# Kernel tuning notes

Measured on AMD Instinct MI355X. Metric: run time of the kernel, lower is better.

## Reference

```python
import jax, jax.numpy as jnp
import numpy as np

EPS = 1e-5

def batchnorm(x, g, b):
    # training-mode BN: batch statistics over (N,H,W), biased variance (matches torch)
    m = x.mean((0, 2, 3), keepdims=True)
    v = ((x - m) ** 2).mean((0, 2, 3), keepdims=True)
    return g[None, :, None, None] * (x - m) * jax.lax.rsqrt(v + EPS) + b[None, :, None, None]


def deform_conv2d(x, offset, mask, weight, bias):
    # torchvision deform_conv2d v2 semantics, stride=1, pad=1, dilation=1, 1 group, 1 offset group
    B, C, H, W = x.shape
    K = 9  # 3x3 kernel
    off = offset.reshape(B, K, 2, H, W)  # interleaved (dy, dx) per kernel tap
    dy, dx = off[:, :, 0], off[:, :, 1]  # [B,K,H,W]
    kr = jnp.arange(3, dtype=x.dtype) - 1.0
    k_y = jnp.repeat(kr, 3)  # [9] kernel row offsets
    k_x = jnp.tile(kr, 3)    # [9] kernel col offsets
    hh = jnp.arange(H, dtype=x.dtype)
    ww = jnp.arange(W, dtype=x.dtype)
    ph = dy + k_y[None, :, None, None] + hh[None, None, :, None]  # [B,K,H,W] sample rows
    pw = dx + k_x[None, :, None, None] + ww[None, None, None, :]  # [B,K,H,W] sample cols
    h0 = jnp.floor(ph); w0 = jnp.floor(pw)
    lh = ph - h0; lw = pw - w0
    h0i = h0.astype(jnp.int32); w0i = w0.astype(jnp.int32)

    def gather(xb, hb, wb):  # xb [C,H,W], hb/wb [K,H,W] -> [C,K,H,W]
        return xb[:, hb, wb]

    def corner(hi, wi, wgt):
        valid = (hi >= 0) & (hi < H) & (wi >= 0) & (wi < W)
        hic = jnp.clip(hi, 0, H - 1); wic = jnp.clip(wi, 0, W - 1)
        v = jax.vmap(gather)(x, hic, wic)  # [B,C,K,H,W]
        return v * (wgt * valid.astype(x.dtype))[:, None]

    samp = (corner(h0i, w0i, (1 - lh) * (1 - lw))
            + corner(h0i, w0i + 1, (1 - lh) * lw)
            + corner(h0i + 1, w0i, lh * (1 - lw))
            + corner(h0i + 1, w0i + 1, lh * lw))  # [B,C,K,H,W]
    samp = samp * mask[:, None]  # modulated (v2) mask [B,1,K,H,W]
    out = jnp.einsum('bckhw,ock->bohw', samp, weight.reshape(weight.shape[0], C, K))
    return out + bias[None, :, None, None]


def reference(x, conv1_w, bn1_g, bn1_b, off_w, off_b, dcn_w, dcn_b, norm_g, norm_b):
    flip = x[..., ::-1]
    xp = batchnorm(jnp.einsum('bchw,oc->bohw', x, conv1_w), bn1_g, bn1_b)  # 1x1 conv + BN, no relu
    concat = jnp.concatenate([flip, xp], axis=1)  # [B,2C,H,W]
    out = jax.lax.conv_general_dilated(concat, off_w, (1, 1), 'SAME',
                                       dimension_numbers=('NCHW', 'OIHW', 'NCHW'))
    out = out + off_b[None, :, None, None]  # [B,27,H,W]
    o1, o2, mask = jnp.split(out, 3, axis=1)
    offset = jnp.concatenate([o1, o2], axis=1)  # [B,18,H,W]
    mask = jax.nn.sigmoid(mask)  # [B,9,H,W]
    d = deform_conv2d(xp, offset, mask, dcn_w, dcn_b)
    return jax.nn.relu(batchnorm(d, norm_g, norm_b) + xp)


def setup_inputs() -> dict:
    key = jax.random.key(0)
    ks = jax.random.split(key, 6)
    B, C, H, W = 8, 256, 45, 80
    stdv = 1.0 / np.sqrt(C * 9)
    return {
        'x': jax.random.normal(ks[0], (B, C, H, W), jnp.float32),
        'conv1_w': jax.random.normal(ks[1], (C, C), jnp.float32) * 0.05,
        'bn1_g': jnp.ones((C,), jnp.float32),
        'bn1_b': jnp.zeros((C,), jnp.float32),
        'off_w': jax.random.normal(ks[2], (27, 2 * C, 3, 3), jnp.float32) * 0.01,
        'off_b': jax.random.normal(ks[3], (27,), jnp.float32) * 0.01,
        'dcn_w': jax.random.uniform(ks[4], (C, C, 3, 3), jnp.float32, -stdv, stdv),
        'dcn_b': jax.random.normal(ks[5], (C,), jnp.float32) * 0.01,
        'norm_g': jnp.ones((C,), jnp.float32),
        'norm_b': jnp.zeros((C,), jnp.float32),
    }
```

## Files before the change

kernel.cpp:

```cpp
#include <hip/hip_runtime.h>
#include <math.h>

#define BATCH 8
#define CH 256
#define HH 45
#define WW 80
#define HW 3600
#define PTOT 28800

typedef unsigned short u16;
typedef unsigned int   u32;
typedef __attribute__((ext_vector_type(8))) short bf16x8;
typedef __attribute__((ext_vector_type(4))) float f32x4;

struct __align__(8) us4 { u16 x, y, z, w; };

__device__ __forceinline__ u16 bf16_rne(float x) {
  u32 u = __float_as_uint(x);
  u += 0x7FFF + ((u >> 16) & 1);
  return (u16)(u >> 16);
}

__global__ __launch_bounds__(256) void prep_wts(
    const float* __restrict__ conv1_w, const float* __restrict__ off_w,
    const float* __restrict__ dcn_w,
    u16* __restrict__ w1b, u16* __restrict__ wt_offb, u16* __restrict__ wt_b)
{
  int i = blockIdx.x * 256 + threadIdx.x;
  if (i < 256 * 256) {
    w1b[i] = bf16_rne(conv1_w[i]);
  }
  if (i < 9 * 32 * 512) {
    int tap = i >> 14;
    int r   = i & 16383;
    int oc  = r >> 9;
    int c   = r & 511;
    float v = (oc < 27) ? off_w[((size_t)oc * 512 + c) * 9 + tap] : 0.f;
    wt_offb[i] = bf16_rne(v);
  }
  if (i < 9 * 256 * 256) {
    int c = i & 255;
    int oc = (i >> 8) & 255;
    int tap = i >> 16;
    wt_b[i] = bf16_rne(dcn_w[((size_t)oc * 256 + c) * 9 + tap]);
  }
}

__global__ __launch_bounds__(256) void flip_transpose(
    const float* __restrict__ x, u16* __restrict__ concat)
{
  __shared__ float tile[32][36];
  const int b  = blockIdx.z;
  const int c0 = blockIdx.y * 32;
  const int p0 = blockIdx.x * 32;
  int rem = HW - p0; if (rem > 32) rem = 32;
  const int t = threadIdx.x;
  {
    int c = t >> 3, p4 = (t & 7) * 4;
    if (p4 < rem) {
      float4 v = *(const float4*)(x + ((size_t)b * CH + c0 + c) * HW + p0 + p4);
      *(float4*)&tile[c][p4] = v;
    }
  }
  __syncthreads();
  {
    int r = t >> 3, cq = (t & 7) * 4;
    if (r < rem) {
      int p = p0 + r;
      int h = p / WW, w = p - h * WW;
      int pf = h * WW + (WW - 1 - w);
      us4 o;
      o.x = bf16_rne(tile[cq + 0][r]);
      o.y = bf16_rne(tile[cq + 1][r]);
      o.z = bf16_rne(tile[cq + 2][r]);
      o.w = bf16_rne(tile[cq + 3][r]);
      *(us4*)(concat + ((size_t)b * HW + pf) * 512 + c0 + cq) = o;
    }
  }
}

__global__ __launch_bounds__(256) void conv1_mfma(
    const u16* __restrict__ concat, const u16* __restrict__ w1b,
    float* __restrict__ out1, float* __restrict__ part_c1)
{
  const int t = threadIdx.x;
  const int wv = t >> 6, lane = t & 63;
  const int lr = lane & 15, lk = lane >> 4;
  const int id = blockIdx.x;
  const int b  = id & 7;
  const int pt = id >> 3;
  const int oc0 = blockIdx.y * 128 + (wv & 1) * 64;
  const int p0  = pt * 128 + (wv >> 1) * 64;

  const u16* bptr[4];
#pragma unroll
  for (int nt = 0; nt < 4; nt++) {
    int pl = p0 + nt * 16 + lr;
    int pc = pl < HW ? pl : HW - 1;
    int h = pc / WW, w = pc - h * WW;
    int pf = b * HW + h * WW + (WW - 1 - w);
    bptr[nt] = concat + (size_t)pf * 512 + lk * 8;
  }
  const u16* aptr = w1b + ((size_t)(oc0 + lr)) * 256 + lk * 8;

  f32x4 acc[4][4];
#pragma unroll
  for (int mt = 0; mt < 4; mt++)
#pragma unroll
    for (int nt = 0; nt < 4; nt++) acc[mt][nt] = (f32x4)0.f;

#pragma unroll
  for (int cc = 0; cc < 8; cc++) {
    bf16x8 af[4], bfv[4];
#pragma unroll
    for (int mt = 0; mt < 4; mt++)
      af[mt] = *(const bf16x8*)(aptr + (size_t)mt * 16 * 256 + cc * 32);
#pragma unroll
    for (int nt = 0; nt < 4; nt++)
      bfv[nt] = *(const bf16x8*)(bptr[nt] + cc * 32);
#pragma unroll
    for (int mt = 0; mt < 4; mt++)
#pragma unroll
      for (int nt = 0; nt < 4; nt++)
        acc[mt][nt] = __builtin_amdgcn_mfma_f32_16x16x32_bf16(
            af[mt], bfv[nt], acc[mt][nt], 0, 0, 0);
  }

#pragma unroll
  for (int mt = 0; mt < 4; mt++) {
    int oc = oc0 + mt * 16 + lk * 4;
#pragma unroll
    for (int nt = 0; nt < 4; nt++) {
      int pl = p0 + nt * 16 + lr;
      if (pl < HW) {
        float* dst = out1 + ((size_t)(b * CH + oc)) * HW + pl;
#pragma unroll
        for (int r = 0; r < 4; r++)
          dst[(size_t)r * HW] = acc[mt][nt][r];
      }
    }
  }

  float sv[4][4], sq[4][4];
#pragma unroll
  for (int mt = 0; mt < 4; mt++)
#pragma unroll
    for (int r = 0; r < 4; r++) { sv[mt][r] = 0.f; sq[mt][r] = 0.f; }
#pragma unroll
  for (int mt = 0; mt < 4; mt++)
#pragma unroll
    for (int nt = 0; nt < 4; nt++) {
      int pl = p0 + nt * 16 + lr;
      if (pl < HW) {
#pragma unroll
        for (int r = 0; r < 4; r++) {
          float v = acc[mt][nt][r];
          sv[mt][r] += v; sq[mt][r] += v * v;
        }
      }
    }
#pragma unroll
  for (int m = 1; m < 16; m <<= 1) {
#pragma unroll
    for (int mt = 0; mt < 4; mt++)
#pragma unroll
      for (int r = 0; r < 4; r++) {
        sv[mt][r] += __shfl_xor(sv[mt][r], m, 64);
        sq[mt][r] += __shfl_xor(sq[mt][r], m, 64);
      }
  }
  if (lr == 0) {
    int slot = (wv >> 1) + 2 * blockIdx.x + 464 * blockIdx.y;
    float* pp = part_c1 + (size_t)slot * 128 * 2;
#pragma unroll
    for (int mt = 0; mt < 4; mt++)
#pragma unroll
      for (int r = 0; r < 4; r++) {
        int ocl = (wv & 1) * 64 + mt * 16 + lk * 4 + r;
        pp[ocl * 2]     = sv[mt][r];
        pp[ocl * 2 + 1] = sq[mt][r];
      }
  }
}

__global__ __launch_bounds__(256) void stats_fin_c1(
    const float* __restrict__ part_c1, float* __restrict__ st)
{
  const int c = blockIdx.x;
  const int y = c >> 7, ocl = c & 127;
  const int t = threadIdx.x;
  const float* base = part_c1 + (size_t)y * 464 * 256 + ocl * 2;
  float s = 0.f, s2 = 0.f;
  for (int i = t; i < 464; i += 256) {
    s  += base[(size_t)i * 256];
    s2 += base[(size_t)i * 256 + 1];
  }
  __shared__ float ls[256], ls2[256];
  ls[t] = s; ls2[t] = s2;
  __syncthreads();
  for (int off = 128; off > 0; off >>= 1) {
    if (t < off) { ls[t] += ls[t + off]; ls2[t] += ls2[t + off]; }
    __syncthreads();
  }
  if (t == 0) {
    float m = ls[0] / (float)PTOT;
    float var = ls2[0] / (float)PTOT - m * m;
    st[c] = m;
    st[CH + c] = rsqrtf(var + 1e-5f);
  }
}

__global__ __launch_bounds__(256) void stats_fin_d(
    const float* __restrict__ part_d, float* __restrict__ st)
{
  const int c = blockIdx.x;
  const int t = threadIdx.x;
  float s = 0.f, s2 = 0.f;
  for (int i = t; i < 456; i += 256) {
    s  += part_d[(size_t)i * 512 + c * 2];
    s2 += part_d[(size_t)i * 512 + c * 2 + 1];
  }
  __shared__ float ls[256], ls2[256];
  ls[t] = s; ls2[t] = s2;
  __syncthreads();
  for (int off = 128; off > 0; off >>= 1) {
    if (t < off) { ls[t] += ls[t + off]; ls2[t] += ls2[t + off]; }
    __syncthreads();
  }
  if (t == 0) {
    float m = ls[0] / (float)PTOT;
    float var = ls2[0] / (float)PTOT - m * m;
    st[c] = m;
    st[CH + c] = rsqrtf(var + 1e-5f);
  }
}

__global__ __launch_bounds__(256) void norm_transpose(
    const float* __restrict__ out1, const float* __restrict__ st,
    const float* __restrict__ g, const float* __restrict__ bb,
    u16* __restrict__ concat)
{
  __shared__ float tile[32][36];
  const int b  = blockIdx.z;
  const int c0 = blockIdx.y * 32;
  const int p0 = blockIdx.x * 32;
  int rem = HW - p0; if (rem > 32) rem = 32;
  const int t = threadIdx.x;

  {
    int c  = t >> 3;
    int p4 = (t & 7) * 4;
    int cg = c0 + c;
    float m  = st[cg], rs = st[CH + cg];
    float sc = g[cg] * rs;
    float sh = bb[cg] - m * sc;
    if (p4 < rem) {
      size_t base = ((size_t)b * CH + cg) * HW + p0;
      float4 v = *(const float4*)(out1 + base + p4);
      v.x = v.x * sc + sh; v.y = v.y * sc + sh;
      v.z = v.z * sc + sh; v.w = v.w * sc + sh;
      *(float4*)&tile[c][p4] = v;
    }
  }
  __syncthreads();
  {
    int r  = t >> 3;
    int cq = (t & 7) * 4;
    if (r < rem) {
      us4 o;
      o.x = bf16_rne(tile[cq + 0][r]);
      o.y = bf16_rne(tile[cq + 1][r]);
      o.z = bf16_rne(tile[cq + 2][r]);
      o.w = bf16_rne(tile[cq + 3][r]);
      *(us4*)(concat + ((size_t)b * HW + p0 + r) * 512 + 256 + c0 + cq) = o;
    }
  }
}

__global__ __launch_bounds__(128) void off_mfma(
    const u16* __restrict__ concat, const u16* __restrict__ wt_offb,
    float* __restrict__ offp3)
{
  const int t = threadIdx.x;
  const int g = blockIdx.y;
  const int wv = t >> 6, lane = t & 63;
  const int lr = lane & 15, lk = lane >> 4;
  const int id = blockIdx.x;
  const int b    = id & 7;
  const int tile = id >> 3;
  int pl = tile * 32 + wv * 16 + lr;
  const bool pvalid = pl < HW;
  if (!pvalid) pl = HW - 1;
  const int P = b * HW + pl;
  const int h = pl / WW, w = pl - h * WW;

  f32x4 acc[2];
  acc[0] = (f32x4)0.f; acc[1] = (f32x4)0.f;

#pragma unroll 1
  for (int tl = 0; tl < 3; tl++) {
    int tap = g * 3 + tl;
    int dy = tap / 3 - 1, dx = tap % 3 - 1;
    bool valid = ((unsigned)(h + dy) < HH) && ((unsigned)(w + dx) < WW);
    int Ps = valid ? (P + dy * WW + dx) : P;
    const u16* bp = concat + (size_t)Ps * 512 + lk * 8;
    const u16* ap = wt_offb + ((size_t)tap * 32 + lr) * 512 + lk * 8;
#pragma unroll
    for (int cc = 0; cc < 16; cc++) {
      bf16x8 bfv = *(const bf16x8*)(bp + cc * 32);
      if (!valid) bfv = (bf16x8)(short)0;
      bf16x8 af0 = *(const bf16x8*)(ap + cc * 32);
      bf16x8 af1 = *(const bf16x8*)(ap + 16 * 512 + cc * 32);
      acc[0] = __builtin_amdgcn_mfma_f32_16x16x32_bf16(af0, bfv, acc[0], 0, 0, 0);
      acc[1] = __builtin_amdgcn_mfma_f32_16x16x32_bf16(af1, bfv, acc[1], 0, 0, 0);
    }
  }

  if (pvalid) {
#pragma unroll
    for (int mt = 0; mt < 2; mt++) {
      int oc = mt * 16 + lk * 4;
#pragma unroll
      for (int r = 0; r < 4; r++)
        offp3[((size_t)g * 32 + oc + r) * PTOT + P] = acc[mt][r];
    }
  }
}

__global__ __launch_bounds__(256) void off_finalize(
    const float* __restrict__ offp3, const float* __restrict__ off_b,
    float4* __restrict__ wts4, int4* __restrict__ idx4)
{
  int i = blockIdx.x * 256 + threadIdx.x;
  if (i >= 9 * PTOT) return;
  int k = i / PTOT;
  int P = i - k * PTOT;
  int b = P / HW;
  int p = P - b * HW;
  int h = p / WW;
  int w = p - h * WW;

  float dy = off_b[2 * k], dx = off_b[2 * k + 1], ml = off_b[18 + k];
#pragma unroll
  for (int g = 0; g < 3; g++) {
    const float* base = offp3 + (size_t)g * 32 * PTOT + P;
    dy += base[(size_t)(2 * k    ) * PTOT];
    dx += base[(size_t)(2 * k + 1) * PTOT];
    ml += base[(size_t)(18 + k   ) * PTOT];
  }

  float m = 1.f / (1.f + expf(-ml));
  float ph = dy + (float)(k / 3 - 1) + (float)h;
  float pw = dx + (float)(k % 3 - 1) + (float)w;
  float h0f = floorf(ph), w0f = floorf(pw);
  float lh = ph - h0f, lw = pw - w0f;
  int h0 = (int)h0f, w0 = (int)w0f;
  int h1 = h0 + 1, w1 = w0 + 1;
  float vh0 = (h0 >= 0 && h0 < HH) ? 1.f : 0.f;
  float vh1 = (h1 >= 0 && h1 < HH) ? 1.f : 0.f;
  float vw0 = (w0 >= 0 && w0 < WW) ? 1.f : 0.f;
  float vw1 = (w1 >= 0 && w1 < WW) ? 1.f : 0.f;
  float4 wv;
  wv.x = (1.f - lh) * (1.f - lw) * m * vh0 * vw0;
  wv.y = (1.f - lh) * lw         * m * vh0 * vw1;
  wv.z = lh * (1.f - lw)         * m * vh1 * vw0;
  wv.w = lh * lw                 * m * vh1 * vw1;
  int hc0 = min(max(h0, 0), HH - 1), hc1 = min(max(h1, 0), HH - 1);
  int wc0 = min(max(w0, 0), WW - 1), wc1 = min(max(w1, 0), WW - 1);
  int base = b * HW;
  int4 iv;
  iv.x = (base + hc0 * WW + wc0) * 512 + 256;
  iv.y = (base + hc0 * WW + wc1) * 512 + 256;
  iv.z = (base + hc1 * WW + wc0) * 512 + 256;
  iv.w = (base + hc1 * WW + wc1) * 512 + 256;
  wts4[i] = wv;
  idx4[i] = iv;
}

__global__ __launch_bounds__(512) void deform_mfma(
    const u16* __restrict__ concat,
    const float4* __restrict__ wts4, const int4* __restrict__ idx4,
    const u16* __restrict__ wt_b,
    float* __restrict__ d, float* __restrict__ part_d)
{
  __shared__ u16   samp[64 * 256];
  __shared__ float4 sw4[64];
  __shared__ int4   sidx4[64];

  const int t    = threadIdx.x;
  const int wv   = t >> 6;
  const int lane = t & 63;
  const int lr = lane & 15, lk = lane >> 4;
  const int id   = blockIdx.x;
  const int b    = id & 7;
  const int tile = id >> 3;
  const int P0   = b * HW + tile * 64;
  int lim  = HW - tile * 64;
  if (lim > 64) lim = 64;

  f32x4 acc[2][4];
#pragma unroll
  for (int mt = 0; mt < 2; mt++)
#pragma unroll
    for (int nt = 0; nt < 4; nt++) acc[mt][nt] = (f32x4)0.f;

  const int c4 = lane * 4;

  for (int tap = 0; tap < 9; tap++) {
    __syncthreads();
    if (t < 64) {
      int off = (t < lim) ? t : (lim - 1);
      sw4[t]   = wts4[(size_t)tap * PTOT + P0 + off];
      sidx4[t] = idx4[(size_t)tap * PTOT + P0 + off];
    }
    __syncthreads();

#pragma unroll 2
    for (int it = 0; it < 8; it++) {
      int pos = it * 8 + wv;
      int4  iv = sidx4[pos];
      float4 wq = sw4[pos];
      uint2 u0 = *(const uint2*)(concat + iv.x + c4);
      uint2 u1 = *(const uint2*)(concat + iv.y + c4);
      uint2 u2 = *(const uint2*)(concat + iv.z + c4);
      uint2 u3 = *(const uint2*)(concat + iv.w + c4);
      float a0, a1, a2, a3;
      a0  = wq.x * __uint_as_float(u0.x << 16);
      a1  = wq.x * __uint_as_float(u0.x & 0xFFFF0000u);
      a2  = wq.x * __uint_as_float(u0.y << 16);
      a3  = wq.x * __uint_as_float(u0.y & 0xFFFF0000u);
      a0 = fmaf(wq.y, __uint_as_float(u1.x << 16), a0);
      a1 = fmaf(wq.y, __uint_as_float(u1.x & 0xFFFF0000u), a1);
      a2 = fmaf(wq.y, __uint_as_float(u1.y << 16), a2);
      a3 = fmaf(wq.y, __uint_as_float(u1.y & 0xFFFF0000u), a3);
      a0 = fmaf(wq.z, __uint_as_float(u2.x << 16), a0);
      a1 = fmaf(wq.z, __uint_as_float(u2.x & 0xFFFF0000u), a1);
      a2 = fmaf(wq.z, __uint_as_float(u2.y << 16), a2);
      a3 = fmaf(wq.z, __uint_as_float(u2.y & 0xFFFF0000u), a3);
      a0 = fmaf(wq.w, __uint_as_float(u3.x << 16), a0);
      a1 = fmaf(wq.w, __uint_as_float(u3.x & 0xFFFF0000u), a1);
      a2 = fmaf(wq.w, __uint_as_float(u3.y << 16), a2);
      a3 = fmaf(wq.w, __uint_as_float(u3.y & 0xFFFF0000u), a3);
      uint2 r;
      r.x = (__float_as_uint(a0) >> 16) | (__float_as_uint(a1) & 0xFFFF0000u);
      r.y = (__float_as_uint(a2) >> 16) | (__float_as_uint(a3) & 0xFFFF0000u);
      u32 byte = (u32)pos * 512u + (u32)c4 * 2u;
      byte ^= (u32)(pos & 7) << 4;
      *(uint2*)((char*)samp + byte) = r;
    }
    __syncthreads();

#pragma unroll 1
    for (int cc = 0; cc < 8; cc++) {
      int c0 = cc * 32;
      bf16x8 bfr[4];
#pragma unroll
      for (int nt = 0; nt < 4; nt++) {
        int pos = nt * 16 + lr;
        u32 byte = (u32)pos * 512u + (u32)(c0 + lk * 8) * 2u;
        byte ^= (u32)(pos & 7) << 4;
        bfr[nt] = *(const bf16x8*)((const char*)samp + byte);
      }
      const u16* wp = wt_b + ((size_t)tap * 256 + wv * 32 + lr) * 256
                      + c0 + lk * 8;
      bf16x8 afr[2];
#pragma unroll
      for (int mt = 0; mt < 2; mt++)
        afr[mt] = *(const bf16x8*)(wp + (size_t)mt * 16 * 256);
#pragma unroll
      for (int mt = 0; mt < 2; mt++)
#pragma unroll
        for (int nt = 0; nt < 4; nt++)
          acc[mt][nt] = __builtin_amdgcn_mfma_f32_16x16x32_bf16(
              afr[mt], bfr[nt], acc[mt][nt], 0, 0, 0);
    }
  }

#pragma unroll
  for (int mt = 0; mt < 2; mt++) {
    int oc = wv * 32 + mt * 16 + lk * 4;
#pragma unroll
    for (int nt = 0; nt < 4; nt++) {
      int pl = tile * 64 + nt * 16 + lr;
      if (pl < HW) {
        float* dst = d + ((size_t)(b * CH + oc)) * HW + pl;
#pragma unroll
        for (int r = 0; r < 4; r++)
          dst[(size_t)r * HW] = acc[mt][nt][r];
      }
    }
  }

  float sv[2][4], sq[2][4];
#pragma unroll
  for (int mt = 0; mt < 2; mt++)
#pragma unroll
    for (int r = 0; r < 4; r++) { sv[mt][r] = 0.f; sq[mt][r] = 0.f; }
#pragma unroll
  for (int mt = 0; mt < 2; mt++)
#pragma unroll
    for (int nt = 0; nt < 4; nt++) {
      int pl = tile * 64 + nt * 16 + lr;
      if (pl < HW) {
#pragma unroll
        for (int r = 0; r < 4; r++) {
          float v = acc[mt][nt][r];
          sv[mt][r] += v; sq[mt][r] += v * v;
        }
      }
    }
#pragma unroll
  for (int m = 1; m < 16; m <<= 1) {
#pragma unroll
    for (int mt = 0; mt < 2; mt++)
#pragma unroll
      for (int r = 0; r < 4; r++) {
        sv[mt][r] += __shfl_xor(sv[mt][r], m, 64);
        sq[mt][r] += __shfl_xor(sq[mt][r], m, 64);
      }
  }
  if (lr == 0) {
    float* pp = part_d + (size_t)blockIdx.x * 512;
#pragma unroll
    for (int mt = 0; mt < 2; mt++)
#pragma unroll
      for (int r = 0; r < 4; r++) {
        int oc = wv * 32 + mt * 16 + lk * 4 + r;
        pp[oc * 2]     = sv[mt][r];
        pp[oc * 2 + 1] = sq[mt][r];
      }
  }
}

__global__ __launch_bounds__(256) void final_nchw(
    const float* __restrict__ d, const float* __restrict__ out1raw,
    const float* __restrict__ st1, const float* __restrict__ g1,
    const float* __restrict__ b1,
    const float* __restrict__ st2, const float* __restrict__ g2,
    const float* __restrict__ b2, float* __restrict__ out)
{
  u32 i4 = blockIdx.x * 256 + threadIdx.x;
  u32 e = i4 * 4;
  int row = (int)(e / HW);
  int c = row & 255;
  float m1 = st1[c], rs1 = st1[CH + c];
  float sc1 = g1[c] * rs1;
  float sh1 = b1[c] - m1 * sc1;
  float m2 = st2[c], rs2 = st2[CH + c];
  float sc2 = g2[c] * rs2;
  float sh2 = b2[c] - m2 * sc2;
  float4 dv = *(const float4*)(d + e);
  float4 xv = *(const float4*)(out1raw + e);
  float4 o;
  o.x = dv.x * sc2 + sh2 + xv.x * sc1 + sh1;
  o.y = dv.y * sc2 + sh2 + xv.y * sc1 + sh1;
  o.z = dv.z * sc2 + sh2 + xv.z * sc1 + sh1;
  o.w = dv.w * sc2 + sh2 + xv.w * sc1 + sh1;
  o.x = o.x > 0.f ? o.x : 0.f;
  o.y = o.y > 0.f ? o.y : 0.f;
  o.z = o.z > 0.f ? o.z : 0.f;
  o.w = o.w > 0.f ? o.w : 0.f;
  *(float4*)(out + e) = o;
}

extern "C" void kernel_launch(void* const* d_in, const int* in_sizes, int n_in,
                              void* d_out, int out_size, void* d_ws, size_t ws_size,
                              hipStream_t stream)
{
  const float* x       = (const float*)d_in[0];
  const float* conv1_w = (const float*)d_in[1];
  const float* bn1_g   = (const float*)d_in[2];
  const float* bn1_b   = (const float*)d_in[3];
  const float* off_w   = (const float*)d_in[4];
  const float* off_b   = (const float*)d_in[5];
  const float* dcn_w   = (const float*)d_in[6];
  const float* norm_g  = (const float*)d_in[8];
  const float* norm_b  = (const float*)d_in[9];
  float* out = (float*)d_out;

  char* ws = (char*)d_ws;
  size_t o = 0;
  float* out1    = (float*)(ws + o); o += (size_t)PTOT * CH * 4;
  u16*   concat  = (u16*)  (ws + o); o += (size_t)PTOT * 512 * 2;
  float* dbuf    = (float*)(ws + o); o += (size_t)PTOT * CH * 4;
  float* offp3   = (float*)(ws + o); o += (size_t)96 * PTOT * 4;
  u16*   wt_b    = (u16*)  (ws + o); o += (size_t)9 * 256 * 256 * 2;
  u16*   wt_offb = (u16*)  (ws + o); o += (size_t)9 * 32 * 512 * 2;
  u16*   w1b     = (u16*)  (ws + o); o += (size_t)256 * 256 * 2;
  float4* wts4   = (float4*)(ws + o); o += (size_t)9 * PTOT * 16;
  int4*   idx4   = (int4*) (ws + o); o += (size_t)9 * PTOT * 16;
  float* st      = (float*)(ws + o); o += 512 * 4;
  float* st2     = (float*)(ws + o); o += 512 * 4;
  float* part_c1 = (float*)(ws + o); o += (size_t)928 * 128 * 2 * 4;
  float* part_d  = (float*)(ws + o); o += (size_t)456 * 512 * 4;

  prep_wts<<<2304, 256, 0, stream>>>(conv1_w, off_w, dcn_w, w1b, wt_offb, wt_b);
  flip_transpose<<<dim3(113, 8, 8), 256, 0, stream>>>(x, concat);
  conv1_mfma<<<dim3(232, 2), 256, 0, stream>>>(concat, w1b, out1, part_c1);
  stats_fin_c1<<<256, 256, 0, stream>>>(part_c1, st);
  norm_transpose<<<dim3(113, 8, 8), 256, 0, stream>>>(out1, st, bn1_g, bn1_b, concat);
  off_mfma<<<dim3(904, 3), 128, 0, stream>>>(concat, wt_offb, offp3);
  off_finalize<<<(9 * PTOT + 255) / 256, 256, 0, stream>>>(offp3, off_b, wts4, idx4);
  deform_mfma<<<456, 512, 0, stream>>>(concat, wts4, idx4, wt_b, dbuf, part_d);
  stats_fin_d<<<256, 256, 0, stream>>>(part_d, st2);
  final_nchw<<<7200, 256, 0, stream>>>(dbuf, out1, st, bn1_g, bn1_b,
                                       st2, norm_g, norm_b, out);
}
```

Before: 274.6 us.

## Fuse weight prep into flip kernel and preload all deform tap metadata

Merges the weight bf16 conversion kernel into the flip/transpose kernel, using the first 2304 blocks of the 7232-block grid, which removes one launch. In the deform kernel, all nine taps' sample indices and bilinear weights are loaded into shared memory once up front. This replaces the two barriers and the global load per tap with one barrier per tap. Shared memory per block grows by about 18KB, which may reduce occupancy.

```diff
diff --git a/kernel.cpp b/kernel.cpp
--- a/kernel.cpp
+++ b/kernel.cpp
@@ -21,33 +21,11 @@
   return (u16)(u >> 16);
 }
 
-__global__ __launch_bounds__(256) void prep_wts(
+__global__ __launch_bounds__(256) void flip_prep(
+    const float* __restrict__ x, u16* __restrict__ concat,
     const float* __restrict__ conv1_w, const float* __restrict__ off_w,
     const float* __restrict__ dcn_w,
     u16* __restrict__ w1b, u16* __restrict__ wt_offb, u16* __restrict__ wt_b)
-{
-  int i = blockIdx.x * 256 + threadIdx.x;
-  if (i < 256 * 256) {
-    w1b[i] = bf16_rne(conv1_w[i]);
-  }
-  if (i < 9 * 32 * 512) {
-    int tap = i >> 14;
-    int r   = i & 16383;
-    int oc  = r >> 9;
-    int c   = r & 511;
-    float v = (oc < 27) ? off_w[((size_t)oc * 512 + c) * 9 + tap] : 0.f;
-    wt_offb[i] = bf16_rne(v);
-  }
-  if (i < 9 * 256 * 256) {
-    int c = i & 255;
-    int oc = (i >> 8) & 255;
-    int tap = i >> 16;
-    wt_b[i] = bf16_rne(dcn_w[((size_t)oc * 256 + c) * 9 + tap]);
-  }
-}
-
-__global__ __launch_bounds__(256) void flip_transpose(
-    const float* __restrict__ x, u16* __restrict__ concat)
 {
   __shared__ float tile[32][36];
   const int b  = blockIdx.z;
@@ -55,6 +33,31 @@
   const int p0 = blockIdx.x * 32;
   int rem = HW - p0; if (rem > 32) rem = 32;
   const int t = threadIdx.x;
+
+  {
+    int linid = blockIdx.x + 113 * (blockIdx.y + 8 * blockIdx.z);
+    if (linid < 2304) {
+      int i = linid * 256 + t;
+      if (i < 256 * 256) {
+        w1b[i] = bf16_rne(conv1_w[i]);
+      }
+      if (i < 9 * 32 * 512) {
+        int tap = i >> 14;
+        int r   = i & 16383;
+        int oc  = r >> 9;
+        int c   = r & 511;
+        float v = (oc < 27) ? off_w[((size_t)oc * 512 + c) * 9 + tap] : 0.f;
+        wt_offb[i] = bf16_rne(v);
+      }
+      if (i < 9 * 256 * 256) {
+        int c = i & 255;
+        int oc = (i >> 8) & 255;
+        int tap = i >> 16;
+        wt_b[i] = bf16_rne(dcn_w[((size_t)oc * 256 + c) * 9 + tap]);
+      }
+    }
+  }
+
   {
     int c = t >> 3, p4 = (t & 7) * 4;
     if (p4 < rem) {
@@ -383,9 +386,9 @@
     const u16* __restrict__ wt_b,
     float* __restrict__ d, float* __restrict__ part_d)
 {
-  __shared__ u16   samp[64 * 256];
-  __shared__ float4 sw4[64];
-  __shared__ int4   sidx4[64];
+  __shared__ u16    samp[64 * 256];
+  __shared__ int4   sidx[9][64];
+  __shared__ float4 swq[9][64];
 
   const int t    = threadIdx.x;
   const int wv   = t >> 6;
@@ -398,6 +401,14 @@
   int lim  = HW - tile * 64;
   if (lim > 64) lim = 64;
 
+  for (int item = t; item < 9 * 64; item += 512) {
+    int tap = item >> 6, pos = item & 63;
+    int off = (pos < lim) ? pos : (lim - 1);
+    sidx[tap][pos] = idx4[(size_t)tap * PTOT + P0 + off];
+    swq[tap][pos]  = wts4[(size_t)tap * PTOT + P0 + off];
+  }
+  __syncthreads();
+
   f32x4 acc[2][4];
 #pragma unroll
   for (int mt = 0; mt < 2; mt++)
@@ -407,19 +418,11 @@
   const int c4 = lane * 4;
 
   for (int tap = 0; tap < 9; tap++) {
-    __syncthreads();
-    if (t < 64) {
-      int off = (t < lim) ? t : (lim - 1);
-      sw4[t]   = wts4[(size_t)tap * PTOT + P0 + off];
-      sidx4[t] = idx4[(size_t)tap * PTOT + P0 + off];
-    }
-    __syncthreads();
-
 #pragma unroll 2
     for (int it = 0; it < 8; it++) {
       int pos = it * 8 + wv;
-      int4  iv = sidx4[pos];
-      float4 wq = sw4[pos];
+      int4  iv = sidx[tap][pos];
+      float4 wq = swq[tap][pos];
       uint2 u0 = *(const uint2*)(concat + iv.x + c4);
       uint2 u1 = *(const uint2*)(concat + iv.y + c4);
       uint2 u2 = *(const uint2*)(concat + iv.z + c4);
@@ -474,6 +477,7 @@
           acc[mt][nt] = __builtin_amdgcn_mfma_f32_16x16x32_bf16(
               afr[mt], bfr[nt], acc[mt][nt], 0, 0, 0);
     }
+    __syncthreads();
   }
 
 #pragma unroll
@@ -594,8 +598,8 @@
   float* part_c1 = (float*)(ws + o); o += (size_t)928 * 128 * 2 * 4;
   float* part_d  = (float*)(ws + o); o += (size_t)456 * 512 * 4;
 
-  prep_wts<<<2304, 256, 0, stream>>>(conv1_w, off_w, dcn_w, w1b, wt_offb, wt_b);
-  flip_transpose<<<dim3(113, 8, 8), 256, 0, stream>>>(x, concat);
+  flip_prep<<<dim3(113, 8, 8), 256, 0, stream>>>(x, concat, conv1_w, off_w,
+                                                 dcn_w, w1b, wt_offb, wt_b);
   conv1_mfma<<<dim3(232, 2), 256, 0, stream>>>(concat, w1b, out1, part_c1);
   stats_fin_c1<<<256, 256, 0, stream>>>(part_c1, st);
   norm_transpose<<<dim3(113, 8, 8), 256, 0, stream>>>(out1, st, bn1_g, bn1_b, concat);
```

After: 270.3 us. No clear change (-1.6%).
